# Kernel optimization log

Measured on AMD Instinct MI355X. Metric: run time of the kernel, lower is better.

## Reference

```python
import jax, jax.numpy as jnp
import numpy as np

N_NODES = 50000
N_EDGES = 800000
D = 64
N_TYPES = 4


def setup_inputs() -> dict:
    key = jax.random.key(0)
    ks = jax.random.split(key, 7)
    x = jax.random.normal(ks[0], (N_NODES, D), dtype=jnp.float32)
    vec = jax.random.normal(ks[1], (N_NODES, 3, D), dtype=jnp.float32)
    node_type = jax.random.randint(ks[2], (N_NODES,), 0, N_TYPES)
    src = jax.random.randint(ks[3], (N_EDGES,), 0, N_NODES)
    dst = jax.random.randint(ks[4], (N_EDGES,), 0, N_NODES)
    # per-node-type conv weights (one scalar-channel and one vector-channel matrix per type)
    W_s = jax.random.normal(ks[5], (N_TYPES, D, D), dtype=jnp.float32) / np.sqrt(D)
    W_v = jax.random.normal(ks[6], (N_TYPES, D, D), dtype=jnp.float32) / np.sqrt(D)
    return {"x": x, "vec\u0065c"[0:3]: vec, "node_type": node_type, "src": src, "dst": dst, "W_s": W_s, "W_v": W_v}


def reference(x, vec, node_type, src, dst, W_s, W_v):
    """HeteroVertexConv: for each node type t, take the in-subgraph (edges whose
    destination is of type t), run a linear message-passing conv, and accumulate
    the result at type-t destination nodes only.
    Returns (srsts, vrsts) = new (data.x, data.vec)."""
    n_nodes = x.shape[0]
    n_types = W_s.shape[0]
    srsts = jnp.zeros_like(x)          # [N, D]
    vrsts = jnp.zeros_like(vec)        # [N, 3, D]
    dst_type = node_type[dst]          # [E] type of each edge's destination
    for t in range(n_types):           # small fixed loop over node types
        emask = (dst_type == t)
        # type-t projection of all node features (equiv. to conv on the in-subgraph)
        proj_s = x @ W_s[t]                                   # [N, D]
        proj_v = jnp.einsum('ncd,de->nce', vec, W_v[t])       # [N, 3, D]
        # per-edge messages, zeroed for edges whose dst is not type t
        msg_s = jnp.where(emask[:, None], proj_s[src], 0.0)           # [E, D]
        msg_v = jnp.where(emask[:, None, None], proj_v[src], 0.0)    # [E, 3, D]
        # scatter-add into destinations; only type-t nodes receive mass
        srsts = srsts + jax.ops.segment_sum(msg_s, dst, num_segments=n_nodes)
        vrsts = vrsts + jax.ops.segment_sum(msg_v, dst, num_segments=n_nodes)
    return srsts, vrsts
```

## Files before the change

### kernel.cpp

```cpp
#include <hip/hip_runtime.h>

#define D 64
#define CAP 64
#define EPB 2048
#define ECAP 6144


typedef float f32x4 __attribute__((ext_vector_type(4)));

__device__ __forceinline__ unsigned bf16rne(float f) {
    unsigned u = __float_as_uint(f);
    return (u + 0x7fffu + ((u >> 16) & 1u)) >> 16;
}
__device__ __forceinline__ float bf_lo(unsigned w) { return __uint_as_float(w << 16); }
__device__ __forceinline__ float bf_hi(unsigned w) { return __uint_as_float(w & 0xffff0000u); }

__device__ __forceinline__ float rdlane(float v, int l) {
    return __uint_as_float(__builtin_amdgcn_readlane(__float_as_uint(v), l));
}

__device__ __forceinline__ void acc8(float (&a)[8], const uint4& v) {
    a[0] += bf_lo(v.x); a[1] += bf_hi(v.x);
    a[2] += bf_lo(v.y); a[3] += bf_hi(v.y);
    a[4] += bf_lo(v.z); a[5] += bf_hi(v.z);
    a[6] += bf_lo(v.w); a[7] += bf_hi(v.w);
}

__global__ __launch_bounds__(256) void k_pack_part(
    const float* __restrict__ x, const float* __restrict__ vec,
    const int* __restrict__ src, const int* __restrict__ dst,
    uint4* __restrict__ packed,
    int* __restrict__ gcur,
    unsigned* __restrict__ bucket,
    int n_edges, int n_nodes, int eb1)
{
    if ((int)blockIdx.x >= eb1) {
        int idx = ((int)blockIdx.x - eb1) * 256 + threadIdx.x;
        if (idx >= n_nodes * 32) return;
        int n = idx >> 5, j = idx & 31;
        int ei = j * 8;
        const float* sp = (ei < 64) ? (x + (size_t)n * 64 + ei)
                                    : (vec + (size_t)n * 192 + (ei - 64));
        f32x4 f0 = __builtin_nontemporal_load((const f32x4*)sp);
        f32x4 f1 = __builtin_nontemporal_load((const f32x4*)(sp + 4));
        uint4 w;
        w.x = bf16rne(f0.x) | (bf16rne(f0.y) << 16);
        w.y = bf16rne(f0.z) | (bf16rne(f0.w) << 16);
        w.z = bf16rne(f1.x) | (bf16rne(f1.y) << 16);
        w.w = bf16rne(f1.z) | (bf16rne(f1.w) << 16);
        packed[idx] = w;
        return;
    }

    __shared__ unsigned stage[EPB];
    __shared__ int h[256], off[256], gbase[256], cur[256], wtot[4];
    int tid = threadIdx.x, lane = tid & 63, wv = tid >> 6;
    h[tid] = 0;
    __syncthreads();

    int e0 = (int)blockIdx.x * EPB;
    int d[8], s[8], b[8];
#pragma unroll
    for (int r = 0; r < 8; ++r) {
        int e = e0 + r * 256 + tid;
        bool v = (e < n_edges);
        d[r] = v ? __builtin_nontemporal_load(dst + e) : 0;
        s[r] = v ? __builtin_nontemporal_load(src + e) : 0;
        b[r] = v ? (d[r] >> 8) : -1;
        if (v) atomicAdd(&h[b[r]], 1);
    }
    __syncthreads();

    int hv = h[tid];
    int inc = hv;
#pragma unroll
    for (int o = 1; o < 64; o <<= 1) { int tv = __shfl_up(inc, o); if (lane >= o) inc += tv; }
    if (lane == 63) wtot[wv] = inc;
    __syncthreads();
    if (tid == 0) { int r = 0; for (int q = 0; q < 4; ++q) { int c = wtot[q]; wtot[q] = r; r += c; } }
    __syncthreads();
    int myoff = inc - hv + wtot[wv];
    off[tid] = myoff;
    cur[tid] = myoff;
    gbase[tid] = (hv > 0) ? atomicAdd(&gcur[tid * 16], hv) : 0;
    __syncthreads();

#pragma unroll
    for (int r = 0; r < 8; ++r) {
        if (b[r] >= 0) {
            int p = atomicAdd(&cur[b[r]], 1);
            stage[p] = ((unsigned)d[r] << 16) | (unsigned)s[r];
        }
    }
    __syncthreads();

    int total = n_edges - e0; if (total > EPB) total = EPB;
    for (int i = tid; i < total; i += 256) {
        unsigned rec = stage[i];
        int t = rec >> 24;
        int dp = gbase[t] + (i - off[t]);
        if (dp < ECAP) bucket[(size_t)t * ECAP + dp] = rec;
    }
}

__global__ __launch_bounds__(256) void k_csr(
    const unsigned* __restrict__ bucket, const int* __restrict__ gcur,
    unsigned short* __restrict__ csr, int* __restrict__ counts,
    int* __restrict__ baseo, int n_nodes, int nb)
{
    __shared__ unsigned short stg[ECAP];
    __shared__ int pf[256], lc[256], wtot[4];
    int tid = threadIdx.x, lane = tid & 63, wv = tid >> 6;
    int b = blockIdx.x;

    pf[tid] = (tid < nb) ? gcur[tid * 16] : 0;
    lc[tid] = 0;
    __syncthreads();

    int pv = pf[tid];
    int inc = pv;
#pragma unroll
    for (int o = 1; o < 64; o <<= 1) { int tv = __shfl_up(inc, o); if (lane >= o) inc += tv; }
    if (lane == 63) wtot[wv] = inc;
    __syncthreads();
    if (tid == 0) { int r = 0; for (int q = 0; q < 4; ++q) { int c = wtot[q]; wtot[q] = r; r += c; } }
    __syncthreads();
    pf[tid] = inc - pv + wtot[wv];
    __syncthreads();
    int ebase = pf[b];
    int cnt = gcur[b * 16]; if (cnt > ECAP) cnt = ECAP;
    int n0 = b << 8;
    int nloc = n_nodes - n0; if (nloc > 256) nloc = 256;
    const unsigned* bp = bucket + (size_t)b * ECAP;

    for (int i = tid; i < cnt; i += 256)
        atomicAdd(&lc[(bp[i] >> 16) & 255], 1);
    __syncthreads();

    int cv = lc[tid];
    int inc2 = cv;
#pragma unroll
    for (int o = 1; o < 64; o <<= 1) { int tv = __shfl_up(inc2, o); if (lane >= o) inc2 += tv; }
    if (lane == 63) wtot[wv] = inc2;
    __syncthreads();
    if (tid == 0) { int r = 0; for (int q = 0; q < 4; ++q) { int c = wtot[q]; wtot[q] = r; r += c; } }
    __syncthreads();
    int nbv = inc2 - cv + wtot[wv];
    if (tid < nloc) { counts[n0 + tid] = cv; baseo[n0 + tid] = ebase + nbv; }
    __syncthreads();
    lc[tid] = nbv;
    __syncthreads();

    for (int i = tid; i < cnt; i += 256) {
        unsigned rec = bp[i];
        int p = atomicAdd(&lc[(rec >> 16) & 255], 1);
        stg[p] = (unsigned short)(rec & 0xFFFFu);
    }
    __syncthreads();

    for (int i = tid; i < cnt; i += 256)
        csr[ebase + i] = stg[i];
}

__global__ __launch_bounds__(256) void k_gather_project(
    const uint4* __restrict__ packed, const int* __restrict__ node_type,
    const float* __restrict__ W_s, const float* __restrict__ W_v,
    const int* __restrict__ counts, const int* __restrict__ baseo,
    const unsigned short* __restrict__ csr,
    float* __restrict__ out_s, float* __restrict__ out_v, int n_nodes)
{
    int wave = threadIdx.x >> 6;
    int lane = threadIdx.x & 63;
    int n = blockIdx.x * 4 + wave;
    if (n >= n_nodes) return;
    int half = lane >> 5, hl = lane & 31;

    int t = node_type[n];
    int cnt = counts[n]; if (cnt > CAP) cnt = CAP;
    int base = baseo[n];
    int myidx = (int)__builtin_nontemporal_load(csr + base + lane);

    float a[8];
#pragma unroll
    for (int i = 0; i < 8; ++i) a[i] = 0.f;

    int k = 0;
    for (; k + 16 <= cnt; k += 16) {
        int s[8]; uint4 w[8];
#pragma unroll
        for (int u = 0; u < 8; ++u) s[u] = __shfl(myidx, k + 2 * u + half);
#pragma unroll
        for (int u = 0; u < 8; ++u) w[u] = packed[(size_t)s[u] * 32 + hl];
#pragma unroll
        for (int u = 0; u < 8; ++u) acc8(a, w[u]);
    }
    for (; k + 8 <= cnt; k += 8) {
        int s0 = __shfl(myidx, k     + half);
        int s1 = __shfl(myidx, k + 2 + half);
        int s2 = __shfl(myidx, k + 4 + half);
        int s3 = __shfl(myidx, k + 6 + half);
        uint4 w0 = packed[(size_t)s0 * 32 + hl];
        uint4 w1 = packed[(size_t)s1 * 32 + hl];
        uint4 w2 = packed[(size_t)s2 * 32 + hl];
        uint4 w3 = packed[(size_t)s3 * 32 + hl];
        acc8(a, w0); acc8(a, w1); acc8(a, w2); acc8(a, w3);
    }
    for (; k + 2 <= cnt; k += 2) {
        int s = __shfl(myidx, k + half);
        uint4 w = packed[(size_t)s * 32 + hl];
        acc8(a, w);
    }
    if (k < cnt) {
        int s = __shfl(myidx, k);
        if (half == 0) { uint4 w = packed[(size_t)s * 32 + hl]; acc8(a, w); }
    }
#pragma unroll
    for (int i = 0; i < 8; ++i) a[i] += __shfl_xor(a[i], 32);

    const float* Ws = W_s + (size_t)t * D * D;
    const float* Wv = W_v + (size_t)t * D * D;
    float ys = 0.f, y0 = 0.f, y1 = 0.f, y2 = 0.f;
#pragma unroll
    for (int g = 0; g < 8; ++g) {
        float ws[8], wv[8];
#pragma unroll
        for (int u = 0; u < 8; ++u) {
            ws[u] = Ws[(g * 8 + u) * D + lane];
            wv[u] = Wv[(g * 8 + u) * D + lane];
        }
#pragma unroll
        for (int u = 0; u < 8; ++u) {
            float as  = rdlane(a[u],      g);
            float av0 = rdlane(a[u],  8 + g);
            float av1 = rdlane(a[u], 16 + g);
            float av2 = rdlane(a[u], 24 + g);
            ys = fmaf(as,  ws[u], ys);
            y0 = fmaf(av0, wv[u], y0);
            y1 = fmaf(av1, wv[u], y1);
            y2 = fmaf(av2, wv[u], y2);
        }
    }
    __builtin_nontemporal_store(ys, &out_s[(size_t)n * D + lane]);
    float* ov = out_v + (size_t)n * 3 * D;
    __builtin_nontemporal_store(y0, &ov[lane]);
    __builtin_nontemporal_store(y1, &ov[D + lane]);
    __builtin_nontemporal_store(y2, &ov[2 * D + lane]);
}

__global__ __launch_bounds__(256) void k_hist(
    const int* __restrict__ dst, int* __restrict__ counts,
    int* __restrict__ pos, int n_edges)
{
    int e = blockIdx.x * 256 + threadIdx.x;
    if (e < n_edges) pos[e] = atomicAdd(&counts[dst[e]], 1);
}
__global__ __launch_bounds__(256) void k_base(
    const int* __restrict__ counts, int* __restrict__ base,
    int* __restrict__ cursor, int n_nodes)
{
    int n = blockIdx.x * 256 + threadIdx.x;
    if (n < n_nodes) base[n] = atomicAdd(cursor, counts[n]);
}
__global__ __launch_bounds__(256) void k_fill(
    const int* __restrict__ src, const int* __restrict__ dst,
    const int* __restrict__ base, const int* __restrict__ pos,
    int* __restrict__ csr, int n_edges)
{
    int e = blockIdx.x * 256 + threadIdx.x;
    if (e < n_edges) csr[base[dst[e]] + pos[e]] = src[e];
}
__global__ __launch_bounds__(256) void k_gather_project_f32(
    const float* __restrict__ x, const float* __restrict__ vec,
    const int* __restrict__ node_type,
    const float* __restrict__ W_s, const float* __restrict__ W_v,
    const int* __restrict__ counts, const int* __restrict__ base,
    const int* __restrict__ csr,
    float* __restrict__ out_s, float* __restrict__ out_v, int n_nodes)
{
    __shared__ float agg[4][4 * D];
    int wave = threadIdx.x >> 6, lane = threadIdx.x & 63;
    int ch = lane >> 4, q = lane & 15;
    int n = blockIdx.x * 4 + wave;
    int cnt = 0, b = 0, t = 0;
    if (n < n_nodes) { cnt = counts[n]; b = base[n]; t = node_type[n]; }
    bool isx = (ch == 0);
    const float4* bp = isx ? (const float4*)x : (const float4*)vec;
    int stride4 = isx ? 16 : 48;
    int off4 = isx ? q : (ch - 1) * 16 + q;
    float4 acc = make_float4(0.f, 0.f, 0.f, 0.f);
    for (int k = 0; k < cnt; ++k) {
        int s = csr[b + k];
        float4 r = bp[(size_t)s * stride4 + off4];
        acc.x += r.x; acc.y += r.y; acc.z += r.z; acc.w += r.w;
    }
    *(float4*)&agg[wave][ch * D + q * 4] = acc;
    __syncthreads();
    if (n >= n_nodes) return;
    const float* Ws = W_s + (size_t)t * D * D;
    const float* Wv = W_v + (size_t)t * D * D;
    const float* a0 = &agg[wave][0];
    float ys = 0.f, y0 = 0.f, y1 = 0.f, y2 = 0.f;
#pragma unroll 8
    for (int i = 0; i < D; ++i) {
        float wsi = Ws[i * D + lane], wvi = Wv[i * D + lane];
        ys = fmaf(a0[i], wsi, ys);
        y0 = fmaf(a0[D + i], wvi, y0);
        y1 = fmaf(a0[2 * D + i], wvi, y1);
        y2 = fmaf(a0[3 * D + i], wvi, y2);
    }
    out_s[(size_t)n * D + lane] = ys;
    float* ov = out_v + (size_t)n * 3 * D;
    ov[lane] = y0; ov[D + lane] = y1; ov[2 * D + lane] = y2;
}

extern "C" void kernel_launch(void* const* d_in, const int* in_sizes, int n_in,
                              void* d_out, int out_size, void* d_ws, size_t ws_size,
                              hipStream_t stream) {
    const float* x         = (const float*)d_in[0];
    const float* vec       = (const float*)d_in[1];
    const int*   node_type = (const int*)d_in[2];
    const int*   src       = (const int*)d_in[3];
    const int*   dst       = (const int*)d_in[4];
    const float* W_s       = (const float*)d_in[5];
    const float* W_v       = (const float*)d_in[6];

    int n_nodes = in_sizes[2];
    int n_edges = in_sizes[3];

    float* out_s = (float*)d_out;
    float* out_v = out_s + (size_t)n_nodes * D;

    int eb = (n_edges + 255) / 256;

    int nb = (n_nodes + 255) >> 8;
    size_t packed_bytes = (size_t)n_nodes * 32 * sizeof(uint4);
    size_t csr_bytes    = ((size_t)n_edges + 64) * sizeof(unsigned short);
    csr_bytes = (csr_bytes + 15) & ~(size_t)15;
    size_t counts_bytes = (size_t)n_nodes * sizeof(int);
    size_t baseo_bytes  = (size_t)n_nodes * sizeof(int);
    size_t gcur_bytes   = 256 * 16 * sizeof(int);
    size_t bucket_bytes = (size_t)256 * ECAP * sizeof(unsigned);
    size_t need_fast = packed_bytes + csr_bytes + counts_bytes
                     + baseo_bytes + gcur_bytes + bucket_bytes;

    if (ws_size >= need_fast && n_nodes <= 65536) {
        char* p = (char*)d_ws;
        uint4*          packed = (uint4*)p;             p += packed_bytes;
        unsigned short* csr16  = (unsigned short*)p;    p += csr_bytes;
        int*            counts = (int*)p;               p += counts_bytes;
        int*            baseo  = (int*)p;               p += baseo_bytes;
        int*            gcur   = (int*)p;               p += gcur_bytes;
        unsigned*       bucket = (unsigned*)p;

        (void)hipMemsetAsync(gcur, 0, gcur_bytes, stream);

        int eb1 = (n_edges + EPB - 1) / EPB;
        int pb  = (n_nodes * 32 + 255) / 256;
        k_pack_part<<<eb1 + pb, 256, 0, stream>>>(
            x, vec, src, dst, packed, gcur, bucket, n_edges, n_nodes, eb1);

        k_csr<<<nb, 256, 0, stream>>>(
            bucket, gcur, csr16, counts, baseo, n_nodes, nb);

        int nb4 = (n_nodes + 3) / 4;
        k_gather_project<<<nb4, 256, 0, stream>>>(
            packed, node_type, W_s, W_v, counts, baseo, csr16,
            out_s, out_v, n_nodes);
        return;
    }

    int* cursor = (int*)d_ws;
    int* counts = cursor + 1;
    int* base   = counts + n_nodes;
    int* pos    = base + n_nodes;
    int* csr    = pos + n_edges;
    int nbf = (n_nodes + 255) / 256;
    int nb4 = (n_nodes + 3) / 4;
    (void)hipMemsetAsync(cursor, 0, (size_t)(1 + n_nodes) * sizeof(int), stream);
    k_hist<<<eb, 256, 0, stream>>>(dst, counts, pos, n_edges);
    k_base<<<nbf, 256, 0, stream>>>(counts, base, cursor, n_nodes);
    k_fill<<<eb, 256, 0, stream>>>(src, dst, base, pos, csr, n_edges);
    k_gather_project_f32<<<nb4, 256, 0, stream>>>(
        x, vec, node_type, W_s, W_v, counts, base, csr, out_s, out_v, n_nodes);
}
```

Before: 223.6 us.

## Fuse pack, CSR build and gather-project into one persistent kernel with grid barriers

Merges the three fast-path kernels into a single persistent kernel of 1024 blocks that grid-strides over each phase and separates the phases with atomic spin grid barriers. The goal is to remove two kernel launch boundaries and their drain and refill gaps. The cost is that residency is capped, since the barrier needs all 1024 blocks co-resident or it deadlocks. Shared-memory use also grows because all phase buffers are live at once, and the spin barriers add overhead.

```diff
diff --git a/kernel.cpp b/kernel.cpp
--- a/kernel.cpp
+++ b/kernel.cpp
@@ -4,6 +4,7 @@
 #define CAP 64
 #define EPB 2048
 #define ECAP 6144
+#define NBLK 1024
 
 
 typedef float f32x4 __attribute__((ext_vector_type(4)));
@@ -26,225 +27,228 @@
     a[6] += bf_lo(v.w); a[7] += bf_hi(v.w);
 }
 
-__global__ __launch_bounds__(256) void k_pack_part(
+__device__ __forceinline__ void gridbar(int* c) {
+    __syncthreads();
+    if (threadIdx.x == 0) {
+        __hip_atomic_fetch_add(c, 1, __ATOMIC_ACQ_REL, __HIP_MEMORY_SCOPE_AGENT);
+        while (__hip_atomic_load(c, __ATOMIC_ACQUIRE, __HIP_MEMORY_SCOPE_AGENT)
+               < (int)gridDim.x)
+            __builtin_amdgcn_s_sleep(8);
+    }
+    __syncthreads();
+}
+
+__global__ __launch_bounds__(256, 4) void k_mega(
     const float* __restrict__ x, const float* __restrict__ vec,
     const int* __restrict__ src, const int* __restrict__ dst,
-    uint4* __restrict__ packed,
-    int* __restrict__ gcur,
-    unsigned* __restrict__ bucket,
-    int n_edges, int n_nodes, int eb1)
-{
-    if ((int)blockIdx.x >= eb1) {
-        int idx = ((int)blockIdx.x - eb1) * 256 + threadIdx.x;
-        if (idx >= n_nodes * 32) return;
-        int n = idx >> 5, j = idx & 31;
-        int ei = j * 8;
-        const float* sp = (ei < 64) ? (x + (size_t)n * 64 + ei)
-                                    : (vec + (size_t)n * 192 + (ei - 64));
-        f32x4 f0 = __builtin_nontemporal_load((const f32x4*)sp);
-        f32x4 f1 = __builtin_nontemporal_load((const f32x4*)(sp + 4));
-        uint4 w;
-        w.x = bf16rne(f0.x) | (bf16rne(f0.y) << 16);
-        w.y = bf16rne(f0.z) | (bf16rne(f0.w) << 16);
-        w.z = bf16rne(f1.x) | (bf16rne(f1.y) << 16);
-        w.w = bf16rne(f1.z) | (bf16rne(f1.w) << 16);
-        packed[idx] = w;
-        return;
-    }
-
+    const int* __restrict__ node_type,
+    const float* __restrict__ W_s, const float* __restrict__ W_v,
+    uint4* __restrict__ packed, int* __restrict__ gcur,
+    unsigned* __restrict__ bucket, unsigned short* __restrict__ csr,
+    int* __restrict__ counts, int* __restrict__ baseo,
+    float* __restrict__ out_s, float* __restrict__ out_v,
+    int* __restrict__ bar,
+    int n_edges, int n_nodes, int eb1, int pb, int nb, int nb4)
+{
     __shared__ unsigned stage[EPB];
     __shared__ int h[256], off[256], gbase[256], cur[256], wtot[4];
-    int tid = threadIdx.x, lane = tid & 63, wv = tid >> 6;
-    h[tid] = 0;
-    __syncthreads();
-
-    int e0 = (int)blockIdx.x * EPB;
-    int d[8], s[8], b[8];
-#pragma unroll
-    for (int r = 0; r < 8; ++r) {
-        int e = e0 + r * 256 + tid;
-        bool v = (e < n_edges);
-        d[r] = v ? __builtin_nontemporal_load(dst + e) : 0;
-        s[r] = v ? __builtin_nontemporal_load(src + e) : 0;
-        b[r] = v ? (d[r] >> 8) : -1;
-        if (v) atomicAdd(&h[b[r]], 1);
-    }
-    __syncthreads();
-
-    int hv = h[tid];
-    int inc = hv;
-#pragma unroll
-    for (int o = 1; o < 64; o <<= 1) { int tv = __shfl_up(inc, o); if (lane >= o) inc += tv; }
-    if (lane == 63) wtot[wv] = inc;
-    __syncthreads();
-    if (tid == 0) { int r = 0; for (int q = 0; q < 4; ++q) { int c = wtot[q]; wtot[q] = r; r += c; } }
-    __syncthreads();
-    int myoff = inc - hv + wtot[wv];
-    off[tid] = myoff;
-    cur[tid] = myoff;
-    gbase[tid] = (hv > 0) ? atomicAdd(&gcur[tid * 16], hv) : 0;
-    __syncthreads();
-
-#pragma unroll
-    for (int r = 0; r < 8; ++r) {
-        if (b[r] >= 0) {
-            int p = atomicAdd(&cur[b[r]], 1);
-            stage[p] = ((unsigned)d[r] << 16) | (unsigned)s[r];
-        }
-    }
-    __syncthreads();
-
-    int total = n_edges - e0; if (total > EPB) total = EPB;
-    for (int i = tid; i < total; i += 256) {
-        unsigned rec = stage[i];
-        int t = rec >> 24;
-        int dp = gbase[t] + (i - off[t]);
-        if (dp < ECAP) bucket[(size_t)t * ECAP + dp] = rec;
-    }
-}
-
-__global__ __launch_bounds__(256) void k_csr(
-    const unsigned* __restrict__ bucket, const int* __restrict__ gcur,
-    unsigned short* __restrict__ csr, int* __restrict__ counts,
-    int* __restrict__ baseo, int n_nodes, int nb)
-{
     __shared__ unsigned short stg[ECAP];
-    __shared__ int pf[256], lc[256], wtot[4];
-    int tid = threadIdx.x, lane = tid & 63, wv = tid >> 6;
-    int b = blockIdx.x;
-
-    pf[tid] = (tid < nb) ? gcur[tid * 16] : 0;
-    lc[tid] = 0;
-    __syncthreads();
-
-    int pv = pf[tid];
-    int inc = pv;
-#pragma unroll
-    for (int o = 1; o < 64; o <<= 1) { int tv = __shfl_up(inc, o); if (lane >= o) inc += tv; }
-    if (lane == 63) wtot[wv] = inc;
-    __syncthreads();
-    if (tid == 0) { int r = 0; for (int q = 0; q < 4; ++q) { int c = wtot[q]; wtot[q] = r; r += c; } }
-    __syncthreads();
-    pf[tid] = inc - pv + wtot[wv];
-    __syncthreads();
-    int ebase = pf[b];
-    int cnt = gcur[b * 16]; if (cnt > ECAP) cnt = ECAP;
-    int n0 = b << 8;
-    int nloc = n_nodes - n0; if (nloc > 256) nloc = 256;
-    const unsigned* bp = bucket + (size_t)b * ECAP;
-
-    for (int i = tid; i < cnt; i += 256)
-        atomicAdd(&lc[(bp[i] >> 16) & 255], 1);
-    __syncthreads();
-
-    int cv = lc[tid];
-    int inc2 = cv;
-#pragma unroll
-    for (int o = 1; o < 64; o <<= 1) { int tv = __shfl_up(inc2, o); if (lane >= o) inc2 += tv; }
-    if (lane == 63) wtot[wv] = inc2;
-    __syncthreads();
-    if (tid == 0) { int r = 0; for (int q = 0; q < 4; ++q) { int c = wtot[q]; wtot[q] = r; r += c; } }
-    __syncthreads();
-    int nbv = inc2 - cv + wtot[wv];
-    if (tid < nloc) { counts[n0 + tid] = cv; baseo[n0 + tid] = ebase + nbv; }
-    __syncthreads();
-    lc[tid] = nbv;
-    __syncthreads();
-
-    for (int i = tid; i < cnt; i += 256) {
-        unsigned rec = bp[i];
-        int p = atomicAdd(&lc[(rec >> 16) & 255], 1);
-        stg[p] = (unsigned short)(rec & 0xFFFFu);
-    }
-    __syncthreads();
-
-    for (int i = tid; i < cnt; i += 256)
-        csr[ebase + i] = stg[i];
-}
-
-__global__ __launch_bounds__(256) void k_gather_project(
-    const uint4* __restrict__ packed, const int* __restrict__ node_type,
-    const float* __restrict__ W_s, const float* __restrict__ W_v,
-    const int* __restrict__ counts, const int* __restrict__ baseo,
-    const unsigned short* __restrict__ csr,
-    float* __restrict__ out_s, float* __restrict__ out_v, int n_nodes)
-{
-    int wave = threadIdx.x >> 6;
-    int lane = threadIdx.x & 63;
-    int n = blockIdx.x * 4 + wave;
-    if (n >= n_nodes) return;
-    int half = lane >> 5, hl = lane & 31;
-
-    int t = node_type[n];
-    int cnt = counts[n]; if (cnt > CAP) cnt = CAP;
-    int base = baseo[n];
-    int myidx = (int)__builtin_nontemporal_load(csr + base + lane);
-
-    float a[8];
-#pragma unroll
-    for (int i = 0; i < 8; ++i) a[i] = 0.f;
-
-    int k = 0;
-    for (; k + 16 <= cnt; k += 16) {
-        int s[8]; uint4 w[8];
-#pragma unroll
-        for (int u = 0; u < 8; ++u) s[u] = __shfl(myidx, k + 2 * u + half);
-#pragma unroll
-        for (int u = 0; u < 8; ++u) w[u] = packed[(size_t)s[u] * 32 + hl];
-#pragma unroll
-        for (int u = 0; u < 8; ++u) acc8(a, w[u]);
-    }
-    for (; k + 8 <= cnt; k += 8) {
-        int s0 = __shfl(myidx, k     + half);
-        int s1 = __shfl(myidx, k + 2 + half);
-        int s2 = __shfl(myidx, k + 4 + half);
-        int s3 = __shfl(myidx, k + 6 + half);
-        uint4 w0 = packed[(size_t)s0 * 32 + hl];
-        uint4 w1 = packed[(size_t)s1 * 32 + hl];
-        uint4 w2 = packed[(size_t)s2 * 32 + hl];
-        uint4 w3 = packed[(size_t)s3 * 32 + hl];
-        acc8(a, w0); acc8(a, w1); acc8(a, w2); acc8(a, w3);
-    }
-    for (; k + 2 <= cnt; k += 2) {
-        int s = __shfl(myidx, k + half);
-        uint4 w = packed[(size_t)s * 32 + hl];
-        acc8(a, w);
-    }
-    if (k < cnt) {
-        int s = __shfl(myidx, k);
-        if (half == 0) { uint4 w = packed[(size_t)s * 32 + hl]; acc8(a, w); }
-    }
-#pragma unroll
-    for (int i = 0; i < 8; ++i) a[i] += __shfl_xor(a[i], 32);
-
-    const float* Ws = W_s + (size_t)t * D * D;
-    const float* Wv = W_v + (size_t)t * D * D;
-    float ys = 0.f, y0 = 0.f, y1 = 0.f, y2 = 0.f;
-#pragma unroll
-    for (int g = 0; g < 8; ++g) {
-        float ws[8], wv[8];
-#pragma unroll
-        for (int u = 0; u < 8; ++u) {
-            ws[u] = Ws[(g * 8 + u) * D + lane];
-            wv[u] = Wv[(g * 8 + u) * D + lane];
-        }
-#pragma unroll
-        for (int u = 0; u < 8; ++u) {
-            float as  = rdlane(a[u],      g);
-            float av0 = rdlane(a[u],  8 + g);
-            float av1 = rdlane(a[u], 16 + g);
-            float av2 = rdlane(a[u], 24 + g);
-            ys = fmaf(as,  ws[u], ys);
-            y0 = fmaf(av0, wv[u], y0);
-            y1 = fmaf(av1, wv[u], y1);
-            y2 = fmaf(av2, wv[u], y2);
-        }
-    }
-    __builtin_nontemporal_store(ys, &out_s[(size_t)n * D + lane]);
-    float* ov = out_v + (size_t)n * 3 * D;
-    __builtin_nontemporal_store(y0, &ov[lane]);
-    __builtin_nontemporal_store(y1, &ov[D + lane]);
-    __builtin_nontemporal_store(y2, &ov[2 * D + lane]);
+    __shared__ int pf[256], lc[256];
+
+    int tid = threadIdx.x, lane = tid & 63;
+
+    for (int vb = blockIdx.x; vb < eb1 + pb; vb += gridDim.x) {
+        if (vb >= eb1) {
+            int idx = (vb - eb1) * 256 + tid;
+            if (idx < n_nodes * 32) {
+                int n = idx >> 5, j = idx & 31;
+                int ei = j * 8;
+                const float* sp = (ei < 64) ? (x + (size_t)n * 64 + ei)
+                                            : (vec + (size_t)n * 192 + (ei - 64));
+                f32x4 f0 = __builtin_nontemporal_load((const f32x4*)sp);
+                f32x4 f1 = __builtin_nontemporal_load((const f32x4*)(sp + 4));
+                uint4 w;
+                w.x = bf16rne(f0.x) | (bf16rne(f0.y) << 16);
+                w.y = bf16rne(f0.z) | (bf16rne(f0.w) << 16);
+                w.z = bf16rne(f1.x) | (bf16rne(f1.y) << 16);
+                w.w = bf16rne(f1.z) | (bf16rne(f1.w) << 16);
+                packed[idx] = w;
+            }
+            continue;
+        }
+        h[tid] = 0;
+        __syncthreads();
+        int e0 = vb * EPB;
+        int d[8], s[8], b[8];
+#pragma unroll
+        for (int r = 0; r < 8; ++r) {
+            int e = e0 + r * 256 + tid;
+            bool v = (e < n_edges);
+            d[r] = v ? __builtin_nontemporal_load(dst + e) : 0;
+            s[r] = v ? __builtin_nontemporal_load(src + e) : 0;
+            b[r] = v ? (d[r] >> 8) : -1;
+            if (v) atomicAdd(&h[b[r]], 1);
+        }
+        __syncthreads();
+        int hv = h[tid];
+        int inc = hv;
+#pragma unroll
+        for (int o = 1; o < 64; o <<= 1) { int tv = __shfl_up(inc, o); if (lane >= o) inc += tv; }
+        if (lane == 63) wtot[tid >> 6] = inc;
+        __syncthreads();
+        if (tid == 0) { int r = 0; for (int q = 0; q < 4; ++q) { int c = wtot[q]; wtot[q] = r; r += c; } }
+        __syncthreads();
+        int myoff = inc - hv + wtot[tid >> 6];
+        off[tid] = myoff;
+        cur[tid] = myoff;
+        gbase[tid] = (hv > 0) ? atomicAdd(&gcur[tid * 16], hv) : 0;
+        __syncthreads();
+#pragma unroll
+        for (int r = 0; r < 8; ++r) {
+            if (b[r] >= 0) {
+                int p = atomicAdd(&cur[b[r]], 1);
+                stage[p] = ((unsigned)d[r] << 16) | (unsigned)s[r];
+            }
+        }
+        __syncthreads();
+        int total = n_edges - e0; if (total > EPB) total = EPB;
+        for (int i = tid; i < total; i += 256) {
+            unsigned rec = stage[i];
+            int t = rec >> 24;
+            int dp = gbase[t] + (i - off[t]);
+            if (dp < ECAP) bucket[(size_t)t * ECAP + dp] = rec;
+        }
+        __syncthreads();
+    }
+
+    gridbar(&bar[0]);
+
+    for (int vb = blockIdx.x; vb < nb; vb += gridDim.x) {
+        int wv = tid >> 6;
+        pf[tid] = (tid < nb) ? gcur[tid * 16] : 0;
+        lc[tid] = 0;
+        __syncthreads();
+        int pv = pf[tid];
+        int inc = pv;
+#pragma unroll
+        for (int o = 1; o < 64; o <<= 1) { int tv = __shfl_up(inc, o); if (lane >= o) inc += tv; }
+        if (lane == 63) wtot[wv] = inc;
+        __syncthreads();
+        if (tid == 0) { int r = 0; for (int q = 0; q < 4; ++q) { int c = wtot[q]; wtot[q] = r; r += c; } }
+        __syncthreads();
+        pf[tid] = inc - pv + wtot[wv];
+        __syncthreads();
+        int ebase = pf[vb];
+        int cnt = gcur[vb * 16]; if (cnt > ECAP) cnt = ECAP;
+        int n0 = vb << 8;
+        int nloc = n_nodes - n0; if (nloc > 256) nloc = 256;
+        const unsigned* bp = bucket + (size_t)vb * ECAP;
+
+        for (int i = tid; i < cnt; i += 256)
+            atomicAdd(&lc[(bp[i] >> 16) & 255], 1);
+        __syncthreads();
+        int cv = lc[tid];
+        int inc2 = cv;
+#pragma unroll
+        for (int o = 1; o < 64; o <<= 1) { int tv = __shfl_up(inc2, o); if (lane >= o) inc2 += tv; }
+        if (lane == 63) wtot[wv] = inc2;
+        __syncthreads();
+        if (tid == 0) { int r = 0; for (int q = 0; q < 4; ++q) { int c = wtot[q]; wtot[q] = r; r += c; } }
+        __syncthreads();
+        int nbv = inc2 - cv + wtot[wv];
+        if (tid < nloc) { counts[n0 + tid] = cv; baseo[n0 + tid] = ebase + nbv; }
+        __syncthreads();
+        lc[tid] = nbv;
+        __syncthreads();
+        for (int i = tid; i < cnt; i += 256) {
+            unsigned rec = bp[i];
+            int p = atomicAdd(&lc[(rec >> 16) & 255], 1);
+            stg[p] = (unsigned short)(rec & 0xFFFFu);
+        }
+        __syncthreads();
+        for (int i = tid; i < cnt; i += 256)
+            csr[ebase + i] = stg[i];
+        __syncthreads();
+    }
+
+    gridbar(&bar[1]);
+
+    for (int vb = blockIdx.x; vb < nb4; vb += gridDim.x) {
+        int n = vb * 4 + (tid >> 6);
+        if (n >= n_nodes) continue;
+        int half = lane >> 5, hl = lane & 31;
+
+        int t = node_type[n];
+        int cnt = counts[n]; if (cnt > CAP) cnt = CAP;
+        int base = baseo[n];
+        int myidx = (int)__builtin_nontemporal_load(csr + base + lane);
+
+        float a[8];
+#pragma unroll
+        for (int i = 0; i < 8; ++i) a[i] = 0.f;
+
+        int k = 0;
+        for (; k + 16 <= cnt; k += 16) {
+            int s[8]; uint4 w[8];
+#pragma unroll
+            for (int u = 0; u < 8; ++u) s[u] = __shfl(myidx, k + 2 * u + half);
+#pragma unroll
+            for (int u = 0; u < 8; ++u) w[u] = packed[(size_t)s[u] * 32 + hl];
+#pragma unroll
+            for (int u = 0; u < 8; ++u) acc8(a, w[u]);
+        }
+        for (; k + 8 <= cnt; k += 8) {
+            int s0 = __shfl(myidx, k     + half);
+            int s1 = __shfl(myidx, k + 2 + half);
+            int s2 = __shfl(myidx, k + 4 + half);
+            int s3 = __shfl(myidx, k + 6 + half);
+            uint4 w0 = packed[(size_t)s0 * 32 + hl];
+            uint4 w1 = packed[(size_t)s1 * 32 + hl];
+            uint4 w2 = packed[(size_t)s2 * 32 + hl];
+            uint4 w3 = packed[(size_t)s3 * 32 + hl];
+            acc8(a, w0); acc8(a, w1); acc8(a, w2); acc8(a, w3);
+        }
+        for (; k + 2 <= cnt; k += 2) {
+            int s = __shfl(myidx, k + half);
+            uint4 w = packed[(size_t)s * 32 + hl];
+            acc8(a, w);
+        }
+        if (k < cnt) {
+            int s = __shfl(myidx, k);
+            if (half == 0) { uint4 w = packed[(size_t)s * 32 + hl]; acc8(a, w); }
+        }
+#pragma unroll
+        for (int i = 0; i < 8; ++i) a[i] += __shfl_xor(a[i], 32);
+
+        const float* Ws = W_s + (size_t)t * D * D;
+        const float* Wv = W_v + (size_t)t * D * D;
+        float ys = 0.f, y0 = 0.f, y1 = 0.f, y2 = 0.f;
+#pragma unroll
+        for (int g = 0; g < 8; ++g) {
+            float ws[8], wv[8];
+#pragma unroll
+            for (int u = 0; u < 8; ++u) {
+                ws[u] = Ws[(g * 8 + u) * D + lane];
+                wv[u] = Wv[(g * 8 + u) * D + lane];
+            }
+#pragma unroll
+            for (int u = 0; u < 8; ++u) {
+                float as  = rdlane(a[u],      g);
+                float av0 = rdlane(a[u],  8 + g);
+                float av1 = rdlane(a[u], 16 + g);
+                float av2 = rdlane(a[u], 24 + g);
+                ys = fmaf(as,  ws[u], ys);
+                y0 = fmaf(av0, wv[u], y0);
+                y1 = fmaf(av1, wv[u], y1);
+                y2 = fmaf(av2, wv[u], y2);
+            }
+        }
+        __builtin_nontemporal_store(ys, &out_s[(size_t)n * D + lane]);
+        float* ov = out_v + (size_t)n * 3 * D;
+        __builtin_nontemporal_store(y0, &ov[lane]);
+        __builtin_nontemporal_store(y1, &ov[D + lane]);
+        __builtin_nontemporal_store(y2, &ov[2 * D + lane]);
+    }
 }
 
 __global__ __launch_bounds__(256) void k_hist(
@@ -339,9 +343,10 @@
     size_t counts_bytes = (size_t)n_nodes * sizeof(int);
     size_t baseo_bytes  = (size_t)n_nodes * sizeof(int);
     size_t gcur_bytes   = 256 * 16 * sizeof(int);
+    size_t bar_bytes    = 64;
     size_t bucket_bytes = (size_t)256 * ECAP * sizeof(unsigned);
     size_t need_fast = packed_bytes + csr_bytes + counts_bytes
-                     + baseo_bytes + gcur_bytes + bucket_bytes;
+                     + baseo_bytes + gcur_bytes + bar_bytes + bucket_bytes;
 
     if (ws_size >= need_fast && n_nodes <= 65536) {
         char* p = (char*)d_ws;
@@ -350,22 +355,20 @@
         int*            counts = (int*)p;               p += counts_bytes;
         int*            baseo  = (int*)p;               p += baseo_bytes;
         int*            gcur   = (int*)p;               p += gcur_bytes;
+        int*            bar    = (int*)p;               p += bar_bytes;
         unsigned*       bucket = (unsigned*)p;
 
-        (void)hipMemsetAsync(gcur, 0, gcur_bytes, stream);
+        (void)hipMemsetAsync(gcur, 0, gcur_bytes + bar_bytes, stream);
 
         int eb1 = (n_edges + EPB - 1) / EPB;
         int pb  = (n_nodes * 32 + 255) / 256;
-        k_pack_part<<<eb1 + pb, 256, 0, stream>>>(
-            x, vec, src, dst, packed, gcur, bucket, n_edges, n_nodes, eb1);
-
-        k_csr<<<nb, 256, 0, stream>>>(
-            bucket, gcur, csr16, counts, baseo, n_nodes, nb);
-
         int nb4 = (n_nodes + 3) / 4;
-        k_gather_project<<<nb4, 256, 0, stream>>>(
-            packed, node_type, W_s, W_v, counts, baseo, csr16,
-            out_s, out_v, n_nodes);
+
+        k_mega<<<NBLK, 256, 0, stream>>>(
+            x, vec, src, dst, node_type, W_s, W_v,
+            packed, gcur, bucket, csr16, counts, baseo,
+            out_s, out_v, bar,
+            n_edges, n_nodes, eb1, pb, nb, nb4);
         return;
     }
 
```

Result: slower. 785.6 us (+251.3%).
